# Kernel optimization log

Measured on AMD Instinct MI355X. Metric: run time of the kernel, lower is better.

## Reference

```python
import jax, jax.numpy as jnp
import numpy as np

# DeepSeek-V2-Lite MoE dims
E = 64      # n_routed_experts
H = 2048    # hidden_size
I = 1408    # moe_intermediate_size
K = 6       # num_experts_per_tok (top-k)
T = 1024    # tokens
C = 256     # per-expert capacity (expected load T*K/E = 96; 256 is ample, no drops with seed 0)


def setup_inputs() -> dict:
    key = jax.random.key(0)
    k1, k2, k3, k4 = jax.random.split(key, 4)
    return {
        "hidden_states": jax.random.normal(k1, (T, H), jnp.float32),
        "gate_w": jax.random.normal(k2, (H, E), jnp.float32) * 0.02,   # LiteLinear(H->E), no bias
        "w1": jax.random.normal(k3, (E, H, I), jnp.float32) * 0.02,    # experts_w1
        "w2": jax.random.normal(k4, (E, I, H), jnp.float32) * 0.02,    # experts_w2
    }


def _moe(x, gate_w, w1, w2):
    # Router: softmax gate + top-k + renormalize (vLLM fused_moe renormalize=True)
    logits = x @ gate_w                                    # [T, E]
    probs = jax.nn.softmax(logits, axis=-1)
    topk_w, topk_idx = jax.lax.top_k(probs, K)             # [T, K]
    topk_w = topk_w / jnp.sum(topk_w, axis=-1, keepdims=True)

    # Dispatch: flatten (token, k) pairs, compute slot position within each expert
    P = T * K
    e_p = topk_idx.reshape(P)                              # expert id per pair
    onehot = (e_p[:, None] == jnp.arange(E)[None, :]).astype(jnp.int32)  # [P, E]
    pos = jnp.cumsum(onehot, axis=0) - 1                   # running count per expert
    pos = jnp.take_along_axis(pos, e_p[:, None], axis=1)[:, 0]           # [P]
    valid = pos < C
    pos_c = jnp.where(valid, pos, 0)
    fvalid = valid[:, None].astype(x.dtype)

    x_pair = jnp.repeat(x, K, axis=0)                      # [P, H]
    xe = jnp.zeros((E, C, H), x.dtype).at[e_p, pos_c].add(x_pair * fvalid)  # [E, C, H]

    # Grouped expert GEMMs: silu(x @ w1) @ w2
    h = jax.nn.silu(jnp.einsum('ech,ehi->eci', xe, w1))    # [E, C, I]
    ye = jnp.einsum('eci,eih->ech', h, w2)                 # [E, C, H]

    # Combine: gather back per pair, weight by routing prob, sum over k
    y_pair = ye[e_p, pos_c] * fvalid                       # [P, H]
    out = (y_pair.reshape(T, K, H) * topk_w[..., None]).sum(axis=1)
    return out


def reference(hidden_states, gate_w, w1, w2):
    return _moe(hidden_states, gate_w, w1, w2)
```

## Files before the change

### kernel.cpp

```cpp
#include <hip/hip_runtime.h>

#define T_TOK 1024
#define H_DIM 2048
#define I_DIM 1408
#define E_NUM 64
#define K_TOP 6
#define CAP   256
#define P_NUM (T_TOK * K_TOP)

typedef __bf16 bf16x8 __attribute__((ext_vector_type(8)));
typedef float  f32x4  __attribute__((ext_vector_type(4)));
typedef unsigned int uint32x2 __attribute__((ext_vector_type(2)));

__device__ inline unsigned pack2bf16(float a, float b) {
    unsigned short au = __builtin_bit_cast(unsigned short, (__bf16)a);
    unsigned short bu = __builtin_bit_cast(unsigned short, (__bf16)b);
    return (unsigned)au | ((unsigned)bu << 16);
}

__device__ inline void wg_barrier() {
    asm volatile("s_waitcnt lgkmcnt(0)" ::: "memory");
    __builtin_amdgcn_s_barrier();
    asm volatile("" ::: "memory");
}

__global__ void zero_out_kernel(float* __restrict__ out) {
    int i = blockIdx.x * 256 + threadIdx.x;
    ((f32x4*)out)[i] = (f32x4){0.f, 0.f, 0.f, 0.f};
}

__global__ __launch_bounds__(256) void router_kernel(
        const float* __restrict__ x, const float* __restrict__ gw,
        float* __restrict__ tw, int* __restrict__ ti, __bf16* __restrict__ xb)
{
    const int t0  = blockIdx.x * 4;
    const int tid = threadIdx.x;
    __shared__ float xs[4][H_DIM];
    __shared__ float part[4][4][E_NUM];

    #pragma unroll
    for (int tt = 0; tt < 4; ++tt) {
        #pragma unroll
        for (int i = 0; i < 8; ++i) {
            float v = x[(size_t)(t0 + tt) * H_DIM + i * 256 + tid];
            xs[tt][i * 256 + tid] = v;
            xb[(size_t)(t0 + tt) * H_DIM + i * 256 + tid] = (__bf16)v;
        }
    }
    __syncthreads();

    const int e = tid & 63, q = tid >> 6;
    float a0 = 0.f, a1 = 0.f, a2 = 0.f, a3 = 0.f;
    for (int hh = q * 512; hh < q * 512 + 512; ++hh) {
        float g = gw[hh * E_NUM + e];
        a0 += xs[0][hh] * g; a1 += xs[1][hh] * g;
        a2 += xs[2][hh] * g; a3 += xs[3][hh] * g;
    }
    part[q][0][e] = a0; part[q][1][e] = a1; part[q][2][e] = a2; part[q][3][e] = a3;
    __syncthreads();

    const int tt = q;
    float l = part[0][tt][e] + part[1][tt][e] + part[2][tt][e] + part[3][tt][e];
    float m = l;
    #pragma unroll
    for (int s = 32; s; s >>= 1) m = fmaxf(m, __shfl_xor(m, s));
    float p = __expf(l - m);
    float sum = p;
    #pragma unroll
    for (int s = 32; s; s >>= 1) sum += __shfl_xor(sum, s);
    float prob = p / sum;

    float v = prob, wsum = 0.f;
    float tv[K_TOP]; int tix[K_TOP];
    #pragma unroll
    for (int k = 0; k < K_TOP; ++k) {
        float bv = v; int bi = e;
        #pragma unroll
        for (int s = 32; s; s >>= 1) {
            float ov = __shfl_xor(bv, s); int oi = __shfl_xor(bi, s);
            if (ov > bv || (ov == bv && oi < bi)) { bv = ov; bi = oi; }
        }
        tv[k] = bv; tix[k] = bi; wsum += bv;
        if (e == bi) v = -1.0f;
    }
    if (e == 0) {
        #pragma unroll
        for (int k = 0; k < K_TOP; ++k) {
            tw[(t0 + tt) * K_TOP + k] = tv[k] / wsum;
            ti[(t0 + tt) * K_TOP + k] = tix[k];
        }
    }
}

__global__ __launch_bounds__(1024) void dispatch_scan_kernel(
        const int* __restrict__ ti, int* __restrict__ cnt,
        int* __restrict__ base, int* __restrict__ list)
{
    __shared__ int lcnt[E_NUM];
    const int tid = threadIdx.x;
    if (tid < E_NUM) lcnt[tid] = 0;
    __syncthreads();
    #pragma unroll
    for (int i = 0; i < P_NUM / 1024; ++i) {
        int p = i * 1024 + tid;
        int e = ti[p];
        int slot = atomicAdd(&lcnt[e], 1);
        if (slot < CAP) list[e * CAP + slot] = p;
    }
    __syncthreads();
    if (tid == 0) {
        int acc = 0;
        for (int e = 0; e < E_NUM; ++e) {
            base[e] = acc;
            int c = lcnt[e];
            cnt[e] = c;
            if (c > CAP) c = CAP;
            acc += (c + 15) & ~15;
        }
    }
}

#define B_LDB 36

__global__ __launch_bounds__(256, 3) void gemm1_kernel(
        const float* __restrict__ w1, const __bf16* __restrict__ xb,
        const int* __restrict__ cnt, const int* __restrict__ base,
        const int* __restrict__ list, __bf16* __restrict__ hbuf)
{
    const int e  = blockIdx.z;
    const int m0 = blockIdx.y * 128;
    const int nb = blockIdx.x * 128;

    int rows = cnt[e]; if (rows > CAP) rows = CAP;
    const int rows_pad = (rows + 15) & ~15;
    if (m0 >= rows_pad) return;
    int mcount = rows_pad - m0; if (mcount > 128) mcount = 128;
    const int nmf = mcount >> 4;
    const int hb = base[e];

    __shared__ __attribute__((aligned(16))) __bf16 As[128][72];
    __shared__ __attribute__((aligned(16))) unsigned Bs[128 * B_LDB];
    __shared__ int ts[128];

    const int tid = threadIdx.x;
    if (tid < 128) {
        int slot = m0 + tid;
        ts[tid] = (slot < rows) ? (list[e * CAP + slot] / K_TOP) : 0;
    }
    __syncthreads();

    const int lane = tid & 63;
    const int wv   = tid >> 6;
    const int l15  = lane & 15;
    const int lg   = lane >> 4;

    const int sm = tid >> 3;
    const int sk = (tid & 7) << 3;
    const __bf16* ap[4];
    #pragma unroll
    for (int it = 0; it < 4; ++it)
        ap[it] = xb + (size_t)ts[it * 32 + sm] * H_DIM + sk;

    const int c4 = tid & 31;
    const int kb = tid >> 5;
    const int Xw = 4 * ((c4 ^ (c4 >> 3)) & 7);
    const float* bload = w1 + (size_t)e * H_DIM * I_DIM + (nb + 4 * c4);

    int cB0 = wv * 32 + l15;
    int cB1 = cB0 + 16;
    int c4r0 = cB0 >> 2, c4r1 = cB1 >> 2;
    const int Xr0 = 4 * ((c4r0 ^ (c4r0 >> 3)) & 7);
    const int Xr1 = 4 * ((c4r1 ^ (c4r1 >> 3)) & 7);
    const unsigned* bfp0 = Bs + cB0 * B_LDB;
    const unsigned* bfp1 = Bs + cB1 * B_LDB;

    f32x4 acc[8][2];
    #pragma unroll
    for (int m = 0; m < 8; ++m) {
        acc[m][0] = (f32x4){0.f, 0.f, 0.f, 0.f};
        acc[m][1] = (f32x4){0.f, 0.f, 0.f, 0.f};
    }

    f32x4 f[8]; bf16x8 av[4];
    {
        const float* bp = bload + (size_t)(4 * kb) * I_DIM;
        #pragma unroll
        for (int r = 0; r < 4; ++r) f[r] = *(const f32x4*)(bp + (size_t)r * I_DIM);
        const float* bp2 = bp + (size_t)32 * I_DIM;
        #pragma unroll
        for (int r = 0; r < 4; ++r) f[4 + r] = *(const f32x4*)(bp2 + (size_t)r * I_DIM);
        #pragma unroll
        for (int it = 0; it < 4; ++it) av[it] = *(const bf16x8*)(ap[it]);
    }

    for (int k0 = 0; k0 < H_DIM; k0 += 64) {
        int kn = k0 + 64; if (kn >= H_DIM) kn = 0;
        wg_barrier();
        #pragma unroll
        for (int it = 0; it < 4; ++it)
            *(bf16x8*)(&As[it * 32 + sm][sk]) = av[it];
        #pragma unroll
        for (int b = 0; b < 2; ++b) {
            #pragma unroll
            for (int i = 0; i < 4; ++i) {
                unsigned lo = pack2bf16(f[4 * b + 0][i], f[4 * b + 1][i]);
                unsigned hi = pack2bf16(f[4 * b + 2][i], f[4 * b + 3][i]);
                int c = 4 * c4 + i;
                int p = 2 * kb + 16 * b;
                *(uint32x2*)(&Bs[c * B_LDB + (p ^ Xw)]) = (uint32x2){lo, hi};
            }
        }
        {
            const float* bp = bload + (size_t)(kn + 4 * kb) * I_DIM;
            #pragma unroll
            for (int r = 0; r < 4; ++r) f[r] = *(const f32x4*)(bp + (size_t)r * I_DIM);
            const float* bp2 = bp + (size_t)32 * I_DIM;
            #pragma unroll
            for (int r = 0; r < 4; ++r) f[4 + r] = *(const f32x4*)(bp2 + (size_t)r * I_DIM);
            #pragma unroll
            for (int it = 0; it < 4; ++it) av[it] = *(const bf16x8*)(ap[it] + kn);
        }
        wg_barrier();
        #pragma unroll
        for (int ks = 0; ks < 2; ++ks) {
            int pbase = ks * 16 + lg * 4;
            bf16x8 b0 = *(const bf16x8*)(bfp0 + (pbase ^ Xr0));
            bf16x8 b1 = *(const bf16x8*)(bfp1 + (pbase ^ Xr1));
            #pragma unroll
            for (int m = 0; m < 8; ++m) {
                if (m < nmf) {
                    bf16x8 a = *(const bf16x8*)(&As[m * 16 + l15][ks * 32 + lg * 8]);
                    acc[m][0] = __builtin_amdgcn_mfma_f32_16x16x32_bf16(a, b0, acc[m][0], 0, 0, 0);
                    acc[m][1] = __builtin_amdgcn_mfma_f32_16x16x32_bf16(a, b1, acc[m][1], 0, 0, 0);
                }
            }
        }
    }

    const int nw = nb + wv * 32;
    #pragma unroll
    for (int m = 0; m < 8; ++m) {
        if (m < nmf) {
            #pragma unroll
            for (int nf = 0; nf < 2; ++nf) {
                #pragma unroll
                for (int j = 0; j < 4; ++j) {
                    int row = m * 16 + lg * 4 + j;
                    int col = nw + nf * 16 + l15;
                    float v = acc[m][nf][j];
                    float s = v / (1.0f + __expf(-v));
                    hbuf[(size_t)(hb + m0 + row) * I_DIM + col] = (__bf16)s;
                }
            }
        }
    }
}

__global__ __launch_bounds__(256, 3) void gemm2_kernel(
        const float* __restrict__ w2, const __bf16* __restrict__ hbuf,
        const int* __restrict__ cnt, const int* __restrict__ base,
        const int* __restrict__ list, const float* __restrict__ tw,
        float* __restrict__ out)
{
    const int e  = blockIdx.z;
    const int m0 = blockIdx.y * 128;
    const int nb = blockIdx.x * 128;

    int rows = cnt[e]; if (rows > CAP) rows = CAP;
    const int rows_pad = (rows + 15) & ~15;
    if (m0 >= rows_pad) return;
    int mcount = rows_pad - m0; if (mcount > 128) mcount = 128;
    const int nmf = mcount >> 4;
    const int hb = base[e];

    __shared__ __attribute__((aligned(16))) __bf16 As[128][72];
    __shared__ __attribute__((aligned(16))) unsigned Bs[128 * B_LDB];
    __shared__ int ps[128];
    __shared__ float tws[128];

    const int tid = threadIdx.x;
    if (tid < 128) {
        int slot = m0 + tid;
        int p = (slot < rows) ? list[e * CAP + slot] : -1;
        ps[tid] = p;
        tws[tid] = (p >= 0) ? tw[p] : 0.f;
    }

    const int lane = tid & 63;
    const int wv   = tid >> 6;
    const int l15  = lane & 15;
    const int lg   = lane >> 4;

    const int sm = tid >> 3;
    const int sk = (tid & 7) << 3;
    const __bf16* abase = hbuf + (size_t)(hb + m0 + sm) * I_DIM + sk;

    const int c4 = tid & 31;
    const int kb = tid >> 5;
    const int Xw = 4 * ((c4 ^ (c4 >> 3)) & 7);
    const float* bload = w2 + (size_t)e * I_DIM * H_DIM + (nb + 4 * c4);

    int cB0 = wv * 32 + l15;
    int cB1 = cB0 + 16;
    int c4r0 = cB0 >> 2, c4r1 = cB1 >> 2;
    const int Xr0 = 4 * ((c4r0 ^ (c4r0 >> 3)) & 7);
    const int Xr1 = 4 * ((c4r1 ^ (c4r1 >> 3)) & 7);
    const unsigned* bfp0 = Bs + cB0 * B_LDB;
    const unsigned* bfp1 = Bs + cB1 * B_LDB;

    f32x4 acc[8][2];
    #pragma unroll
    for (int m = 0; m < 8; ++m) {
        acc[m][0] = (f32x4){0.f, 0.f, 0.f, 0.f};
        acc[m][1] = (f32x4){0.f, 0.f, 0.f, 0.f};
    }

    f32x4 f[8]; bf16x8 av[4];
    {
        const float* bp = bload + (size_t)(4 * kb) * H_DIM;
        #pragma unroll
        for (int r = 0; r < 4; ++r) f[r] = *(const f32x4*)(bp + (size_t)r * H_DIM);
        const float* bp2 = bp + (size_t)32 * H_DIM;
        #pragma unroll
        for (int r = 0; r < 4; ++r) f[4 + r] = *(const f32x4*)(bp2 + (size_t)r * H_DIM);
        #pragma unroll
        for (int it = 0; it < 4; ++it)
            av[it] = *(const bf16x8*)(abase + (size_t)(it * 32) * I_DIM);
    }

    for (int k0 = 0; k0 < I_DIM; k0 += 64) {
        int kn = k0 + 64; if (kn >= I_DIM) kn = 0;
        wg_barrier();
        #pragma unroll
        for (int it = 0; it < 4; ++it)
            *(bf16x8*)(&As[it * 32 + sm][sk]) = av[it];
        #pragma unroll
        for (int b = 0; b < 2; ++b) {
            #pragma unroll
            for (int i = 0; i < 4; ++i) {
                unsigned lo = pack2bf16(f[4 * b + 0][i], f[4 * b + 1][i]);
                unsigned hi = pack2bf16(f[4 * b + 2][i], f[4 * b + 3][i]);
                int c = 4 * c4 + i;
                int p = 2 * kb + 16 * b;
                *(uint32x2*)(&Bs[c * B_LDB + (p ^ Xw)]) = (uint32x2){lo, hi};
            }
        }
        {
            const float* bp = bload + (size_t)(kn + 4 * kb) * H_DIM;
            #pragma unroll
            for (int r = 0; r < 4; ++r) f[r] = *(const f32x4*)(bp + (size_t)r * H_DIM);
            const float* bp2 = bp + (size_t)32 * H_DIM;
            #pragma unroll
            for (int r = 0; r < 4; ++r) f[4 + r] = *(const f32x4*)(bp2 + (size_t)r * H_DIM);
            #pragma unroll
            for (int it = 0; it < 4; ++it)
                av[it] = *(const bf16x8*)(abase + (size_t)(it * 32) * I_DIM + kn);
        }
        wg_barrier();

        #pragma unroll
        for (int ks = 0; ks < 2; ++ks) {
            int pbase = ks * 16 + lg * 4;
            bf16x8 b0 = *(const bf16x8*)(bfp0 + (pbase ^ Xr0));
            bf16x8 b1 = *(const bf16x8*)(bfp1 + (pbase ^ Xr1));
            #pragma unroll
            for (int m = 0; m < 8; ++m) {
                if (m < nmf) {
                    bf16x8 a = *(const bf16x8*)(&As[m * 16 + l15][ks * 32 + lg * 8]);
                    acc[m][0] = __builtin_amdgcn_mfma_f32_16x16x32_bf16(a, b0, acc[m][0], 0, 0, 0);
                    acc[m][1] = __builtin_amdgcn_mfma_f32_16x16x32_bf16(a, b1, acc[m][1], 0, 0, 0);
                }
            }
        }
    }

    const int nw = nb + wv * 32;
    #pragma unroll
    for (int m = 0; m < 8; ++m) {
        if (m < nmf) {
            #pragma unroll
            for (int nf = 0; nf < 2; ++nf) {
                #pragma unroll
                for (int j = 0; j < 4; ++j) {
                    int row = m * 16 + lg * 4 + j;
                    int p = ps[row];
                    if (p >= 0) {
                        int t = p / K_TOP;
                        float v = acc[m][nf][j] * tws[row];
                        atomicAdd(&out[(size_t)t * H_DIM + (nw + nf * 16 + l15)], v);
                    }
                }
            }
        }
    }
}

extern "C" void kernel_launch(void* const* d_in, const int* in_sizes, int n_in,
                              void* d_out, int out_size, void* d_ws, size_t ws_size,
                              hipStream_t stream) {
    const float* x  = (const float*)d_in[0];
    const float* gw = (const float*)d_in[1];
    const float* w1 = (const float*)d_in[2];
    const float* w2 = (const float*)d_in[3];
    float* out = (float*)d_out;

    char* ws = (char*)d_ws;
    int*    cnt  = (int*)ws;
    int*    base = (int*)(ws + 256);
    int*    list = (int*)(ws + 512);
    float*  tw   = (float*)(ws + 66048);
    int*    ti   = (int*)(ws + 90624);
    __bf16* xb   = (__bf16*)(ws + 131072);
    __bf16* hbuf = (__bf16*)(ws + 4325376);

    hipLaunchKernelGGL(zero_out_kernel, dim3(T_TOK * H_DIM / 4 / 256), dim3(256), 0, stream, out);
    hipLaunchKernelGGL(router_kernel, dim3(T_TOK / 4), dim3(256), 0, stream,
                       x, gw, tw, ti, xb);
    hipLaunchKernelGGL(dispatch_scan_kernel, dim3(1), dim3(1024), 0, stream,
                       ti, cnt, base, list);
    hipLaunchKernelGGL(gemm1_kernel, dim3(I_DIM / 128, 2, E_NUM), dim3(256), 0, stream,
                       w1, xb, cnt, base, list, hbuf);
    hipLaunchKernelGGL(gemm2_kernel, dim3(H_DIM / 128, 2, E_NUM), dim3(256), 0, stream,
                       w2, hbuf, cnt, base, list, tw, out);
}
```

Measured before the change: 447.2 us.

## Widen gemm2 N tile to 256 with a 2x2 wave layout

Doubles the gemm2 output tile width from 128 to 256 columns and reorganizes the four waves into a 2x2 grid, each computing 64 rows by 128 columns. Each thread now loads 16 rows of w2 and writes the B tile to LDS with 128-bit stores, and A fragments are reused across 8 N fragments. The aim is higher MFMA work per LDS read, less redundant reloading of the hbuf A tile, and fewer blocks. In exchange, register pressure rises (occupancy hint drops from 3 to 2), LDS use doubles, and wave rows beyond the expert's real row count go idle on lightly loaded experts.

```diff
diff --git a/kernel.cpp b/kernel.cpp
--- a/kernel.cpp
+++ b/kernel.cpp
@@ -11,6 +11,7 @@
 typedef __bf16 bf16x8 __attribute__((ext_vector_type(8)));
 typedef float  f32x4  __attribute__((ext_vector_type(4)));
 typedef unsigned int uint32x2 __attribute__((ext_vector_type(2)));
+typedef unsigned int uint32x4 __attribute__((ext_vector_type(4)));
 
 __device__ inline unsigned pack2bf16(float a, float b) {
     unsigned short au = __builtin_bit_cast(unsigned short, (__bf16)a);
@@ -256,7 +257,7 @@
     }
 }
 
-__global__ __launch_bounds__(256, 3) void gemm2_kernel(
+__global__ __launch_bounds__(256, 2) void gemm2_kernel(
         const float* __restrict__ w2, const __bf16* __restrict__ hbuf,
         const int* __restrict__ cnt, const int* __restrict__ base,
         const int* __restrict__ list, const float* __restrict__ tw,
@@ -264,7 +265,7 @@
 {
     const int e  = blockIdx.z;
     const int m0 = blockIdx.y * 128;
-    const int nb = blockIdx.x * 128;
+    const int nb = blockIdx.x * 256;
 
     int rows = cnt[e]; if (rows > CAP) rows = CAP;
     const int rows_pad = (rows + 15) & ~15;
@@ -274,7 +275,7 @@
     const int hb = base[e];
 
     __shared__ __attribute__((aligned(16))) __bf16 As[128][72];
-    __shared__ __attribute__((aligned(16))) unsigned Bs[128 * B_LDB];
+    __shared__ __attribute__((aligned(16))) unsigned Bs[256 * B_LDB];
     __shared__ int ps[128];
     __shared__ float tws[128];
 
@@ -290,43 +291,33 @@
     const int wv   = tid >> 6;
     const int l15  = lane & 15;
     const int lg   = lane >> 4;
+    const int wm   = wv >> 1;
+    const int wn   = wv & 1;
 
     const int sm = tid >> 3;
     const int sk = (tid & 7) << 3;
     const __bf16* abase = hbuf + (size_t)(hb + m0 + sm) * I_DIM + sk;
 
-    const int c4 = tid & 31;
-    const int kb = tid >> 5;
+    const int c4 = tid & 63;
+    const int kq = tid >> 6;
     const int Xw = 4 * ((c4 ^ (c4 >> 3)) & 7);
-    const float* bload = w2 + (size_t)e * I_DIM * H_DIM + (nb + 4 * c4);
-
-    int cB0 = wv * 32 + l15;
-    int cB1 = cB0 + 16;
-    int c4r0 = cB0 >> 2, c4r1 = cB1 >> 2;
-    const int Xr0 = 4 * ((c4r0 ^ (c4r0 >> 3)) & 7);
-    const int Xr1 = 4 * ((c4r1 ^ (c4r1 >> 3)) & 7);
-    const unsigned* bfp0 = Bs + cB0 * B_LDB;
-    const unsigned* bfp1 = Bs + cB1 * B_LDB;
-
-    f32x4 acc[8][2];
-    #pragma unroll
-    for (int m = 0; m < 8; ++m) {
-        acc[m][0] = (f32x4){0.f, 0.f, 0.f, 0.f};
-        acc[m][1] = (f32x4){0.f, 0.f, 0.f, 0.f};
-    }
-
-    f32x4 f[8]; bf16x8 av[4];
-    {
-        const float* bp = bload + (size_t)(4 * kb) * H_DIM;
-        #pragma unroll
-        for (int r = 0; r < 4; ++r) f[r] = *(const f32x4*)(bp + (size_t)r * H_DIM);
-        const float* bp2 = bp + (size_t)32 * H_DIM;
-        #pragma unroll
-        for (int r = 0; r < 4; ++r) f[4 + r] = *(const f32x4*)(bp2 + (size_t)r * H_DIM);
-        #pragma unroll
-        for (int it = 0; it < 4; ++it)
-            av[it] = *(const bf16x8*)(abase + (size_t)(it * 32) * I_DIM);
-    }
+    const float* bload = w2 + (size_t)e * I_DIM * H_DIM
+                            + (size_t)(16 * kq) * H_DIM + (nb + 4 * c4);
+
+    f32x4 acc[4][8];
+    #pragma unroll
+    for (int m = 0; m < 4; ++m)
+        #pragma unroll
+        for (int nf = 0; nf < 8; ++nf)
+            acc[m][nf] = (f32x4){0.f, 0.f, 0.f, 0.f};
+
+    f32x4 f[16]; bf16x8 av[4];
+    #pragma unroll
+    for (int r = 0; r < 16; ++r)
+        f[r] = *(const f32x4*)(bload + (size_t)r * H_DIM);
+    #pragma unroll
+    for (int it = 0; it < 4; ++it)
+        av[it] = *(const bf16x8*)(abase + (size_t)(it * 32) * I_DIM);
 
     for (int k0 = 0; k0 < I_DIM; k0 += 64) {
         int kn = k0 + 64; if (kn >= I_DIM) kn = 0;
@@ -335,59 +326,63 @@
         for (int it = 0; it < 4; ++it)
             *(bf16x8*)(&As[it * 32 + sm][sk]) = av[it];
         #pragma unroll
-        for (int b = 0; b < 2; ++b) {
-            #pragma unroll
-            for (int i = 0; i < 4; ++i) {
-                unsigned lo = pack2bf16(f[4 * b + 0][i], f[4 * b + 1][i]);
-                unsigned hi = pack2bf16(f[4 * b + 2][i], f[4 * b + 3][i]);
-                int c = 4 * c4 + i;
-                int p = 2 * kb + 16 * b;
-                *(uint32x2*)(&Bs[c * B_LDB + (p ^ Xw)]) = (uint32x2){lo, hi};
-            }
+        for (int i = 0; i < 4; ++i) {
+            int c = 4 * c4 + i;
+            uint32x4 q0, q1;
+            #pragma unroll
+            for (int r = 0; r < 4; ++r)
+                q0[r] = pack2bf16(f[2 * r][i], f[2 * r + 1][i]);
+            #pragma unroll
+            for (int r = 0; r < 4; ++r)
+                q1[r] = pack2bf16(f[8 + 2 * r][i], f[9 + 2 * r][i]);
+            *(uint32x4*)(&Bs[c * B_LDB + ((8 * kq) ^ Xw)])     = q0;
+            *(uint32x4*)(&Bs[c * B_LDB + ((8 * kq + 4) ^ Xw)]) = q1;
         }
         {
-            const float* bp = bload + (size_t)(kn + 4 * kb) * H_DIM;
-            #pragma unroll
-            for (int r = 0; r < 4; ++r) f[r] = *(const f32x4*)(bp + (size_t)r * H_DIM);
-            const float* bp2 = bp + (size_t)32 * H_DIM;
-            #pragma unroll
-            for (int r = 0; r < 4; ++r) f[4 + r] = *(const f32x4*)(bp2 + (size_t)r * H_DIM);
+            const float* bp = bload + (size_t)kn * H_DIM;
+            #pragma unroll
+            for (int r = 0; r < 16; ++r)
+                f[r] = *(const f32x4*)(bp + (size_t)r * H_DIM);
             #pragma unroll
             for (int it = 0; it < 4; ++it)
                 av[it] = *(const bf16x8*)(abase + (size_t)(it * 32) * I_DIM + kn);
         }
         wg_barrier();
-
         #pragma unroll
         for (int ks = 0; ks < 2; ++ks) {
             int pbase = ks * 16 + lg * 4;
-            bf16x8 b0 = *(const bf16x8*)(bfp0 + (pbase ^ Xr0));
-            bf16x8 b1 = *(const bf16x8*)(bfp1 + (pbase ^ Xr1));
-            #pragma unroll
-            for (int m = 0; m < 8; ++m) {
-                if (m < nmf) {
-                    bf16x8 a = *(const bf16x8*)(&As[m * 16 + l15][ks * 32 + lg * 8]);
-                    acc[m][0] = __builtin_amdgcn_mfma_f32_16x16x32_bf16(a, b0, acc[m][0], 0, 0, 0);
-                    acc[m][1] = __builtin_amdgcn_mfma_f32_16x16x32_bf16(a, b1, acc[m][1], 0, 0, 0);
+            bf16x8 a[4];
+            #pragma unroll
+            for (int m = 0; m < 4; ++m)
+                a[m] = *(const bf16x8*)(&As[wm * 64 + m * 16 + l15][ks * 32 + lg * 8]);
+            #pragma unroll
+            for (int nf = 0; nf < 8; ++nf) {
+                int col = wn * 128 + nf * 16 + l15;
+                int c4r = col >> 2;
+                int Xr = 4 * ((c4r ^ (c4r >> 3)) & 7);
+                bf16x8 b = *(const bf16x8*)(&Bs[col * B_LDB + (pbase ^ Xr)]);
+                #pragma unroll
+                for (int m = 0; m < 4; ++m) {
+                    if (wm * 4 + m < nmf)
+                        acc[m][nf] = __builtin_amdgcn_mfma_f32_16x16x32_bf16(a[m], b, acc[m][nf], 0, 0, 0);
                 }
             }
         }
     }
 
-    const int nw = nb + wv * 32;
-    #pragma unroll
-    for (int m = 0; m < 8; ++m) {
-        if (m < nmf) {
-            #pragma unroll
-            for (int nf = 0; nf < 2; ++nf) {
+    #pragma unroll
+    for (int m = 0; m < 4; ++m) {
+        if (wm * 4 + m < nmf) {
+            #pragma unroll
+            for (int nf = 0; nf < 8; ++nf) {
                 #pragma unroll
                 for (int j = 0; j < 4; ++j) {
-                    int row = m * 16 + lg * 4 + j;
+                    int row = wm * 64 + m * 16 + lg * 4 + j;
                     int p = ps[row];
                     if (p >= 0) {
                         int t = p / K_TOP;
                         float v = acc[m][nf][j] * tws[row];
-                        atomicAdd(&out[(size_t)t * H_DIM + (nw + nf * 16 + l15)], v);
+                        atomicAdd(&out[(size_t)t * H_DIM + (nb + wn * 128 + nf * 16 + l15)], v);
                     }
                 }
             }
@@ -420,6 +415,6 @@
                        ti, cnt, base, list);
     hipLaunchKernelGGL(gemm1_kernel, dim3(I_DIM / 128, 2, E_NUM), dim3(256), 0, stream,
                        w1, xb, cnt, base, list, hbuf);
-    hipLaunchKernelGGL(gemm2_kernel, dim3(H_DIM / 128, 2, E_NUM), dim3(256), 0, stream,
+    hipLaunchKernelGGL(gemm2_kernel, dim3(H_DIM / 256, 2, E_NUM), dim3(256), 0, stream,
                        w2, hbuf, cnt, base, list, tw, out);
 }
```

Result: no change. 446.0 us (-0.3%).

## Double-buffer fp32 weight prefetch two K-steps ahead with nontemporal loads in expert GEMMs

Applied to the files above, without the earlier changes.

Both grouped GEMM kernels now keep two register sets of fp32 weight fragments and issue global loads two K-steps ahead, unrolling the main loop by two. Weight loads use nontemporal hints to avoid polluting cache with streamed weights, and the barrier helper swaps its memory clobber for sched_barrier fences. This is meant to hide HBM latency on the weight stream, at the cost of doubled prefetch registers, which may hurt occupancy under launch_bounds(256,3). A missing __syncthreads after the gemm2 ps/tws fill is also added.

```diff
diff --git a/kernel.cpp b/kernel.cpp
--- a/kernel.cpp
+++ b/kernel.cpp
@@ -19,9 +19,10 @@
 }
 
 __device__ inline void wg_barrier() {
-    asm volatile("s_waitcnt lgkmcnt(0)" ::: "memory");
+    __builtin_amdgcn_sched_barrier(0);
+    asm volatile("s_waitcnt lgkmcnt(0)");
     __builtin_amdgcn_s_barrier();
-    asm volatile("" ::: "memory");
+    __builtin_amdgcn_sched_barrier(0);
 }
 
 __global__ void zero_out_kernel(float* __restrict__ out) {
@@ -122,6 +123,47 @@
 
 #define B_LDB 36
 
+#define B_PUBLISH(FREG)                                                         \
+    _Pragma("unroll")                                                           \
+    for (int b = 0; b < 2; ++b) {                                               \
+        _Pragma("unroll")                                                       \
+        for (int i = 0; i < 4; ++i) {                                           \
+            unsigned lo = pack2bf16(FREG[4 * b + 0][i], FREG[4 * b + 1][i]);    \
+            unsigned hi = pack2bf16(FREG[4 * b + 2][i], FREG[4 * b + 3][i]);    \
+            int c = 4 * c4 + i;                                                 \
+            int p = 2 * kb + 16 * b;                                            \
+            *(uint32x2*)(&Bs[c * B_LDB + (p ^ Xw)]) = (uint32x2){lo, hi};       \
+        }                                                                       \
+    }
+
+#define B_ISSUE(FREG, KOFF, LD)                                                 \
+    {                                                                           \
+        const float* bp = bload + (size_t)((KOFF) + 4 * kb) * (LD);             \
+        _Pragma("unroll")                                                       \
+        for (int r = 0; r < 4; ++r)                                             \
+            FREG[r] = __builtin_nontemporal_load((const f32x4*)(bp + (size_t)r * (LD))); \
+        const float* bp2 = bp + (size_t)32 * (LD);                              \
+        _Pragma("unroll")                                                       \
+        for (int r = 0; r < 4; ++r)                                             \
+            FREG[4 + r] = __builtin_nontemporal_load((const f32x4*)(bp2 + (size_t)r * (LD))); \
+    }
+
+#define MFMA_STEP()                                                             \
+    _Pragma("unroll")                                                           \
+    for (int ks = 0; ks < 2; ++ks) {                                            \
+        int pbase = ks * 16 + lg * 4;                                           \
+        bf16x8 b0 = *(const bf16x8*)(bfp0 + (pbase ^ Xr0));                     \
+        bf16x8 b1 = *(const bf16x8*)(bfp1 + (pbase ^ Xr1));                     \
+        _Pragma("unroll")                                                       \
+        for (int m = 0; m < 8; ++m) {                                           \
+            if (m < nmf) {                                                      \
+                bf16x8 a = *(const bf16x8*)(&As[m * 16 + l15][ks * 32 + lg * 8]); \
+                acc[m][0] = __builtin_amdgcn_mfma_f32_16x16x32_bf16(a, b0, acc[m][0], 0, 0, 0); \
+                acc[m][1] = __builtin_amdgcn_mfma_f32_16x16x32_bf16(a, b1, acc[m][1], 0, 0, 0); \
+            }                                                                   \
+        }                                                                       \
+    }
+
 __global__ __launch_bounds__(256, 3) void gemm1_kernel(
         const float* __restrict__ w1, const __bf16* __restrict__ xb,
         const int* __restrict__ cnt, const int* __restrict__ base,
@@ -181,60 +223,40 @@
         acc[m][1] = (f32x4){0.f, 0.f, 0.f, 0.f};
     }
 
-    f32x4 f[8]; bf16x8 av[4];
-    {
-        const float* bp = bload + (size_t)(4 * kb) * I_DIM;
-        #pragma unroll
-        for (int r = 0; r < 4; ++r) f[r] = *(const f32x4*)(bp + (size_t)r * I_DIM);
-        const float* bp2 = bp + (size_t)32 * I_DIM;
-        #pragma unroll
-        for (int r = 0; r < 4; ++r) f[4 + r] = *(const f32x4*)(bp2 + (size_t)r * I_DIM);
-        #pragma unroll
-        for (int it = 0; it < 4; ++it) av[it] = *(const bf16x8*)(ap[it]);
-    }
-
-    for (int k0 = 0; k0 < H_DIM; k0 += 64) {
-        int kn = k0 + 64; if (kn >= H_DIM) kn = 0;
+    f32x4 f0[8], f1[8]; bf16x8 av[4];
+    B_ISSUE(f0, 0, I_DIM)
+    B_ISSUE(f1, 64, I_DIM)
+    #pragma unroll
+    for (int it = 0; it < 4; ++it) av[it] = *(const bf16x8*)(ap[it]);
+
+    const int NSTEP = H_DIM / 64;
+    for (int t = 0; t < NSTEP; t += 2) {
         wg_barrier();
         #pragma unroll
         for (int it = 0; it < 4; ++it)
             *(bf16x8*)(&As[it * 32 + sm][sk]) = av[it];
-        #pragma unroll
-        for (int b = 0; b < 2; ++b) {
-            #pragma unroll
-            for (int i = 0; i < 4; ++i) {
-                unsigned lo = pack2bf16(f[4 * b + 0][i], f[4 * b + 1][i]);
-                unsigned hi = pack2bf16(f[4 * b + 2][i], f[4 * b + 3][i]);
-                int c = 4 * c4 + i;
-                int p = 2 * kb + 16 * b;
-                *(uint32x2*)(&Bs[c * B_LDB + (p ^ Xw)]) = (uint32x2){lo, hi};
-            }
-        }
+        B_PUBLISH(f0)
         {
-            const float* bp = bload + (size_t)(kn + 4 * kb) * I_DIM;
-            #pragma unroll
-            for (int r = 0; r < 4; ++r) f[r] = *(const f32x4*)(bp + (size_t)r * I_DIM);
-            const float* bp2 = bp + (size_t)32 * I_DIM;
-            #pragma unroll
-            for (int r = 0; r < 4; ++r) f[4 + r] = *(const f32x4*)(bp2 + (size_t)r * I_DIM);
-            #pragma unroll
-            for (int it = 0; it < 4; ++it) av[it] = *(const bf16x8*)(ap[it] + kn);
-        }
-        wg_barrier();
-        #pragma unroll
-        for (int ks = 0; ks < 2; ++ks) {
-            int pbase = ks * 16 + lg * 4;
-            bf16x8 b0 = *(const bf16x8*)(bfp0 + (pbase ^ Xr0));
-            bf16x8 b1 = *(const bf16x8*)(bfp1 + (pbase ^ Xr1));
-            #pragma unroll
-            for (int m = 0; m < 8; ++m) {
-                if (m < nmf) {
-                    bf16x8 a = *(const bf16x8*)(&As[m * 16 + l15][ks * 32 + lg * 8]);
-                    acc[m][0] = __builtin_amdgcn_mfma_f32_16x16x32_bf16(a, b0, acc[m][0], 0, 0, 0);
-                    acc[m][1] = __builtin_amdgcn_mfma_f32_16x16x32_bf16(a, b1, acc[m][1], 0, 0, 0);
-                }
-            }
-        }
+            int ka = (t + 1) * 64;
+            #pragma unroll
+            for (int it = 0; it < 4; ++it) av[it] = *(const bf16x8*)(ap[it] + ka);
+            if (t + 2 < NSTEP) B_ISSUE(f0, (t + 2) * 64, I_DIM)
+        }
+        wg_barrier();
+        MFMA_STEP()
+        wg_barrier();
+        #pragma unroll
+        for (int it = 0; it < 4; ++it)
+            *(bf16x8*)(&As[it * 32 + sm][sk]) = av[it];
+        B_PUBLISH(f1)
+        {
+            int ka = (t + 2 < NSTEP) ? (t + 2) * 64 : 0;
+            #pragma unroll
+            for (int it = 0; it < 4; ++it) av[it] = *(const bf16x8*)(ap[it] + ka);
+            if (t + 3 < NSTEP) B_ISSUE(f1, (t + 3) * 64, I_DIM)
+        }
+        wg_barrier();
+        MFMA_STEP()
     }
 
     const int nw = nb + wv * 32;
@@ -285,6 +307,7 @@
         ps[tid] = p;
         tws[tid] = (p >= 0) ? tw[p] : 0.f;
     }
+    __syncthreads();
 
     const int lane = tid & 63;
     const int wv   = tid >> 6;
@@ -315,63 +338,43 @@
         acc[m][1] = (f32x4){0.f, 0.f, 0.f, 0.f};
     }
 
-    f32x4 f[8]; bf16x8 av[4];
-    {
-        const float* bp = bload + (size_t)(4 * kb) * H_DIM;
-        #pragma unroll
-        for (int r = 0; r < 4; ++r) f[r] = *(const f32x4*)(bp + (size_t)r * H_DIM);
-        const float* bp2 = bp + (size_t)32 * H_DIM;
-        #pragma unroll
-        for (int r = 0; r < 4; ++r) f[4 + r] = *(const f32x4*)(bp2 + (size_t)r * H_DIM);
-        #pragma unroll
-        for (int it = 0; it < 4; ++it)
-            av[it] = *(const bf16x8*)(abase + (size_t)(it * 32) * I_DIM);
-    }
-
-    for (int k0 = 0; k0 < I_DIM; k0 += 64) {
-        int kn = k0 + 64; if (kn >= I_DIM) kn = 0;
+    f32x4 f0[8], f1[8]; bf16x8 av[4];
+    B_ISSUE(f0, 0, H_DIM)
+    B_ISSUE(f1, 64, H_DIM)
+    #pragma unroll
+    for (int it = 0; it < 4; ++it)
+        av[it] = *(const bf16x8*)(abase + (size_t)(it * 32) * I_DIM);
+
+    const int NSTEP = I_DIM / 64;
+    for (int t = 0; t < NSTEP; t += 2) {
         wg_barrier();
         #pragma unroll
         for (int it = 0; it < 4; ++it)
             *(bf16x8*)(&As[it * 32 + sm][sk]) = av[it];
-        #pragma unroll
-        for (int b = 0; b < 2; ++b) {
-            #pragma unroll
-            for (int i = 0; i < 4; ++i) {
-                unsigned lo = pack2bf16(f[4 * b + 0][i], f[4 * b + 1][i]);
-                unsigned hi = pack2bf16(f[4 * b + 2][i], f[4 * b + 3][i]);
-                int c = 4 * c4 + i;
-                int p = 2 * kb + 16 * b;
-                *(uint32x2*)(&Bs[c * B_LDB + (p ^ Xw)]) = (uint32x2){lo, hi};
-            }
-        }
+        B_PUBLISH(f0)
         {
-            const float* bp = bload + (size_t)(kn + 4 * kb) * H_DIM;
-            #pragma unroll
-            for (int r = 0; r < 4; ++r) f[r] = *(const f32x4*)(bp + (size_t)r * H_DIM);
-            const float* bp2 = bp + (size_t)32 * H_DIM;
-            #pragma unroll
-            for (int r = 0; r < 4; ++r) f[4 + r] = *(const f32x4*)(bp2 + (size_t)r * H_DIM);
+            int ka = (t + 1) * 64;
             #pragma unroll
             for (int it = 0; it < 4; ++it)
-                av[it] = *(const bf16x8*)(abase + (size_t)(it * 32) * I_DIM + kn);
-        }
-        wg_barrier();
-
-        #pragma unroll
-        for (int ks = 0; ks < 2; ++ks) {
-            int pbase = ks * 16 + lg * 4;
-            bf16x8 b0 = *(const bf16x8*)(bfp0 + (pbase ^ Xr0));
-            bf16x8 b1 = *(const bf16x8*)(bfp1 + (pbase ^ Xr1));
-            #pragma unroll
-            for (int m = 0; m < 8; ++m) {
-                if (m < nmf) {
-                    bf16x8 a = *(const bf16x8*)(&As[m * 16 + l15][ks * 32 + lg * 8]);
-                    acc[m][0] = __builtin_amdgcn_mfma_f32_16x16x32_bf16(a, b0, acc[m][0], 0, 0, 0);
-                    acc[m][1] = __builtin_amdgcn_mfma_f32_16x16x32_bf16(a, b1, acc[m][1], 0, 0, 0);
-                }
-            }
-        }
+                av[it] = *(const bf16x8*)(abase + (size_t)(it * 32) * I_DIM + ka);
+            if (t + 2 < NSTEP) B_ISSUE(f0, (t + 2) * 64, H_DIM)
+        }
+        wg_barrier();
+        MFMA_STEP()
+        wg_barrier();
+        #pragma unroll
+        for (int it = 0; it < 4; ++it)
+            *(bf16x8*)(&As[it * 32 + sm][sk]) = av[it];
+        B_PUBLISH(f1)
+        {
+            int ka = (t + 2 < NSTEP) ? (t + 2) * 64 : 0;
+            #pragma unroll
+            for (int it = 0; it < 4; ++it)
+                av[it] = *(const bf16x8*)(abase + (size_t)(it * 32) * I_DIM + ka);
+            if (t + 3 < NSTEP) B_ISSUE(f1, (t + 3) * 64, H_DIM)
+        }
+        wg_barrier();
+        MFMA_STEP()
     }
 
     const int nw = nb + wv * 32;
@@ -385,9 +388,9 @@
                     int row = m * 16 + lg * 4 + j;
                     int p = ps[row];
                     if (p >= 0) {
-                        int t = p / K_TOP;
+                        int t2 = p / K_TOP;
                         float v = acc[m][nf][j] * tws[row];
-                        atomicAdd(&out[(size_t)t * H_DIM + (nw + nf * 16 + l15)], v);
+                        atomicAdd(&out[(size_t)t2 * H_DIM + (nw + nf * 16 + l15)], v);
                     }
                 }
             }
```

Result: slower. 520.4 us (+16.4%).
